# Kernel optimization log

Measured on AMD Instinct MI355X. Metric: run time of the kernel, lower is better.

The kernel has to match this reference:

```python
import jax, jax.numpy as jnp
import numpy as np

IGNORE_THR = 0.6
CONF_THR = 0.5
MAX_OBJ = 50


def iou(gx, gy, gl, gw, bx, by, bl, bw):
    # Faithful translation of get_ious (broadcastable).
    min_x = jnp.minimum(gx - gl / 2.0, bx - bl / 2.0)
    max_x = jnp.maximum(gx + gl / 2.0, bx + bl / 2.0)
    min_y = jnp.minimum(gy - gw / 2.0, by - bw / 2.0)
    max_y = jnp.maximum(gy + gw / 2.0, by + bw / 2.0)
    union_w = max_y - min_y
    union_h = max_x - min_x
    inter_w = gw + bw - union_w
    inter_l = gl + bl - union_h
    inter = jnp.where((inter_w <= 0) | (inter_l <= 0), 0.0, inter_w * inter_l)
    union = gw * gl + bw * bl - inter
    return inter / union


def build_targets(targets, fmap_preds, anchors, H, W, C):
    B, O, _ = targets.shape
    A = anchors.shape[0]
    # object loop breaks at first class==0 -> cumulative validity
    valid_all = jnp.cumprod((targets[:, :, 0] != 0).astype(jnp.int32), axis=1).astype(bool)  # [B,O]
    bidx = jnp.arange(B)
    aidx = jnp.arange(A)
    ch = jnp.arange(7 + C)

    def step(carry, xs):
        mask, conf, ts, n_gt, n_cor = carry
        t, valid = xs  # t: [B,7], valid: [B]
        gx = t[:, 1] * H
        gy = t[:, 2] * W
        gl = t[:, 3] * H
        gw = t[:, 4] * W
        # anchor matching: centered boxes (0,0,gl,gw) vs (0,0,al,aw) -> [B,A]
        ious = iou(0.0, 0.0, gl[:, None], gw[:, None],
                   0.0, 0.0, anchors[None, :, 0], anchors[None, :, 1])
        a = jnp.argmax(ious, axis=1)
        ax = gx.astype(jnp.int32)
        ay = gy.astype(jnp.int32)
        # conf_mask[b, ious>ign, ax, ay] = 0
        cur = conf[bidx[:, None], aidx[None, :], ax[:, None], ay[:, None]]  # [B,A]
        conf = conf.at[bidx[:, None], aidx[None, :], ax[:, None], ay[:, None]].set(
            jnp.where(valid[:, None] & (ious > IGNORE_THR), False, cur))
        # conf_mask[b, a, ax, ay] = 1 ; mask[b, a, ax, ay] = 1
        conf = conf.at[bidx, a, ax, ay].set(jnp.where(valid, True, conf[bidx, a, ax, ay]))
        mask = mask.at[bidx, a, ax, ay].set(jnp.where(valid, True, mask[bidx, a, ax, ay]))
        vals7 = jnp.stack([gx - ax, gy - ay,
                           jnp.log(gl / anchors[a, 0]), jnp.log(gw / anchors[a, 1]),
                           t[:, 5], t[:, 6], jnp.ones_like(gx)], axis=1)  # [B,7]
        cur_ts = ts[bidx, a, ax, ay]  # [B,7+C]
        cls_id = t[:, 0].astype(jnp.int32)
        new_ts = jnp.where(ch[None, :] < 7,
                           jnp.concatenate([vals7, jnp.zeros((B, C), vals7.dtype)], axis=1),
                           jnp.where(ch[None, :] == 7 + cls_id[:, None], 1.0, cur_ts))
        ts = ts.at[bidx, a, ax, ay].set(jnp.where(valid[:, None], new_ts, cur_ts))
        # statistics
        pred = fmap_preds[bidx, a, ax, ay]  # [B,8]
        piou = iou(gx, gy, gl, gw, pred[:, 0], pred[:, 1], pred[:, 2], pred[:, 3])
        correct = valid & (piou > 0.5) & (pred[:, 6] > CONF_THR)
        return (mask, conf, ts,
                n_gt + valid.astype(jnp.int32).sum(),
                n_cor + correct.astype(jnp.int32).sum()), None

    init = (jnp.zeros((B, A, H, W), bool), jnp.ones((B, A, H, W), bool),
            jnp.zeros((B, A, H, W, 7 + C), jnp.float32), jnp.int32(0), jnp.int32(0))
    xs = (jnp.swapaxes(targets, 0, 1), jnp.swapaxes(valid_all, 0, 1))
    (mask, conf, ts, n_gt, n_cor), _ = jax.lax.scan(step, init, xs)
    # torch uint8: false_mask = conf_mask - mask, truthy iff conf_mask != mask (wraps to 255)
    false_mask = conf != mask
    return ts, mask, false_mask, n_gt, n_cor


def region_loss(output, targets, anchors):
    B, _, H, W = output.shape
    A = anchors.shape[0]
    C = output.shape[1] // A - 7
    out = output.reshape(B, A, 7 + C, H, W).transpose(0, 1, 3, 4, 2)  # [B,A,H,W,7+C]
    o_x = jax.nn.sigmoid(out[..., 0])
    o_y = jax.nn.sigmoid(out[..., 1])
    o_l = out[..., 2]
    o_w = out[..., 3]
    o_im = out[..., 4]
    o_re = out[..., 5]
    o_conf = jax.nn.sigmoid(out[..., 6])
    o_cls = jax.nn.sigmoid(out[..., 7:])

    # get_fmap_prediction: c_x[h,w]=h, c_y[h,w]=w
    c_x = jnp.arange(H, dtype=out.dtype)[None, None, :, None]
    c_y = jnp.arange(W, dtype=out.dtype)[None, None, None, :]
    p_l = anchors[None, :, None, None, 0]
    p_w = anchors[None, :, None, None, 1]
    cls_scalar = jnp.argmax(o_cls).astype(out.dtype)  # scalar, as in original
    fmap_preds = jnp.stack([
        o_x + c_x, o_y + c_y,
        jnp.exp(o_l) * p_l, jnp.exp(o_w) * p_w,
        o_im, o_re, o_conf,
        jnp.broadcast_to(cls_scalar, o_x.shape)], axis=-1)  # [B,A,H,W,8]

    ts, mask, false_mask, n_gt, n_cor = build_targets(
        jax.lax.stop_gradient(targets),
        jax.lax.stop_gradient(fmap_preds),
        jax.lax.stop_gradient(anchors), H, W, C)
    ts = jax.lax.stop_gradient(ts)

    m = mask.astype(out.dtype)
    fm = false_mask.astype(out.dtype)
    nt = jnp.sum(m)
    nf = jnp.sum(fm)

    def mmse(o, t):
        return jnp.sum(m * (o - t) ** 2) / nt

    def bce(p, t, w, n):
        lp = jnp.clip(jnp.log(p), -100.0)
        ln = jnp.clip(jnp.log(1.0 - p), -100.0)
        return jnp.sum(w * -(t * lp + (1.0 - t) * ln)) / n

    loss_x = mmse(o_x, ts[..., 0])
    loss_y = mmse(o_y, ts[..., 1])
    loss_l = mmse(o_l, ts[..., 2])
    loss_w = mmse(o_w, ts[..., 3])
    loss_im = mmse(o_im, ts[..., 4])
    loss_re = mmse(o_re, ts[..., 5])
    loss_conf = bce(o_conf, ts[..., 6], fm, nf) + bce(o_conf, ts[..., 6], m, nt)
    labels = jnp.argmax(ts[..., 7:], axis=-1)
    ce = jax.nn.logsumexp(o_cls, axis=-1) - jnp.take_along_axis(o_cls, labels[..., None], axis=-1)[..., 0]
    loss_cls = (1.0 / B) * jnp.sum(m * ce) / nt
    loss = loss_x + loss_y + loss_w + loss_l + loss_im + loss_re + loss_conf + loss_cls
    return loss, n_gt, n_cor


def setup_inputs() -> dict:
    B, A, C, H, W, O = 32, 5, 8, 96, 96, MAX_OBJ
    key = jax.random.key(0)
    k1, k2, k3, k4, k5, k6 = jax.random.split(key, 6)
    output = jax.random.normal(k1, (B, A * (7 + C), H, W), dtype=jnp.float32)
    cls_all = jax.random.randint(k2, (B, O), 1, C).astype(jnp.float32)
    n_obj = jax.random.randint(k3, (B,), 5, O)
    cls_col = jnp.where(jnp.arange(O)[None, :] < n_obj[:, None], cls_all, 0.0)
    xy = jax.random.uniform(k4, (B, O, 2), minval=0.0, maxval=1.0)
    lw = jax.random.uniform(k5, (B, O, 2), minval=0.02, maxval=0.5)
    imre = jax.random.uniform(k6, (B, O, 2), minval=-1.0, maxval=1.0)
    targets = jnp.concatenate([cls_col[..., None], xy, lw, imre], axis=-1).astype(jnp.float32)
    anchors = jnp.asarray([[1.08, 1.19], [3.42, 4.41], [6.63, 11.38],
                           [9.42, 5.11], [16.62, 10.52]], dtype=jnp.float32)
    return {"output": output, "targets": targets, "anchors": anchors}


def reference(output, targets, anchors):
    return region_loss(output, targets, anchors)
```

## Files before the change

kernel.cpp:

```cpp
#include <hip/hip_runtime.h>

#define Bn 32
#define An 5
#define Cn 8
#define Hn 96
#define Wn 96
#define On 50
#define CHn 15
#define HWn (Hn*Wn)
#define NCELL (Bn*An*HWn)
#define NQ (NCELL/4)
#define QPP (HWn/4)

#define NBLK_D 224
#define GRID1 (Bn + NBLK_D)

#define OFF_BPART 0
#define OFF_PART  (Bn*13*4)

__device__ __forceinline__ float sigmoidf_(float x) { return 1.0f / (1.0f + expf(-x)); }
__device__ __forceinline__ float sp100(float v) {
    return fminf(log1pf(expf(v)), 100.0f);
}

__device__ __forceinline__ float iou_ref(float gx, float gy, float gl, float gw,
                                         float bx, float by, float bl, float bw) {
    float min_x = fminf(gx - gl * 0.5f, bx - bl * 0.5f);
    float max_x = fmaxf(gx + gl * 0.5f, bx + bl * 0.5f);
    float min_y = fminf(gy - gw * 0.5f, by - bw * 0.5f);
    float max_y = fmaxf(gy + gw * 0.5f, by + bw * 0.5f);
    float union_w = max_y - min_y;
    float union_h = max_x - min_x;
    float inter_w = gw + bw - union_w;
    float inter_l = gl + bl - union_h;
    float inter = (inter_w <= 0.0f || inter_l <= 0.0f) ? 0.0f : inter_w * inter_l;
    float uni = gw * gl + bw * bl - inter;
    return inter / uni;
}

__global__ __launch_bounds__(256) void k_main(const float* __restrict__ outp,
                                              const float* __restrict__ tgt,
                                              const float* __restrict__ anch,
                                              float* __restrict__ bpart,
                                              float* __restrict__ partials) {
    const int blk = blockIdx.x;
    const int tid = threadIdx.x;

    if (blk >= Bn) {
        float s = 0.0f;
        for (int q = (blk - Bn) * 256 + tid; q < NQ; q += NBLK_D * 256) {
            int plane = q / QPP;
            int r = q - plane * QPP;
            const float4 v = *(const float4*)(outp + ((size_t)plane * CHn + 6) * HWn + (size_t)r * 4);
            s += sp100(v.x) + sp100(v.y) + sp100(v.z) + sp100(v.w);
        }
        __shared__ float red[256];
        red[tid] = s;
        __syncthreads();
        for (int off = 128; off > 0; off >>= 1) {
            if (tid < off) red[tid] += red[tid + off];
            __syncthreads();
        }
        if (tid == 0) partials[blk - Bn] = red[0];
        return;
    }

    if (tid >= 64) return;
    const int b = blk;
    const int o = tid;

    float anv[10];
    #pragma unroll
    for (int k = 0; k < 10; ++k) anv[k] = anch[k];

    const float* t = tgt + (size_t)(b * On + o) * 7;
    float t0 = (o < On) ? t[0] : 0.0f;
    unsigned long long vm = __ballot(t0 != 0.0f);
    int nv = __ffsll(~vm) - 1;
    bool valid = o < nv;

    int best = 0, ign = 0, cellxy = -1, cls = 0;
    float ef0 = 0, ef1 = 0, ef2 = 0, ef3 = 0, ef4 = 0, ef5 = 0;
    float o0 = 0, o1 = 0, o2 = 0, o3 = 0, o4 = 0, o5 = 0, o6 = 0;
    bool correct = false;
    if (valid) {
        float gx = t[1] * (float)Hn, gy = t[2] * (float)Wn;
        float gl = t[3] * (float)Hn, gw = t[4] * (float)Wn;
        float bi = -1.0f, al = anv[0], aw = anv[1];
        #pragma unroll
        for (int a = 0; a < An; ++a) {
            float ia = iou_ref(0.0f, 0.0f, gl, gw, 0.0f, 0.0f, anv[2 * a], anv[2 * a + 1]);
            if (ia > bi) { bi = ia; best = a; al = anv[2 * a]; aw = anv[2 * a + 1]; }
            if (ia > 0.6f) ign |= (1 << a);
        }
        int ax = (int)gx, ay = (int)gy;
        cellxy = ax * Wn + ay;
        ef0 = gx - (float)ax;
        ef1 = gy - (float)ay;
        ef2 = logf(gl / al);
        ef3 = logf(gw / aw);
        ef4 = t[5];
        ef5 = t[6];
        cls = (int)t0;
        const float* p = outp + ((size_t)(b * An + best) * CHn) * HWn + cellxy;
        o0 = p[0]; o1 = p[HWn]; o2 = p[2 * HWn]; o3 = p[3 * HWn];
        o4 = p[4 * HWn]; o5 = p[5 * HWn]; o6 = p[6 * HWn];
        float px = sigmoidf_(o0) + (float)ax;
        float py = sigmoidf_(o1) + (float)ay;
        float pl = expf(o2) * al;
        float pw = expf(o3) * aw;
        float pc = sigmoidf_(o6);
        float piou = iou_ref(gx, gy, gl, gw, px, py, pl, pw);
        correct = (piou > 0.5f) && (pc > 0.5f);
    }
    int ncor = __popcll(__ballot(correct));

    int keyt = best * HWn + cellxy;
    bool has_later = false, has_earlier = false;
    int clsmin = cls, cbits = 0x1F, mbits = 0;
    for (int j = 0; j < nv; ++j) {
        int jc = __shfl(cellxy, j);
        int jb = __shfl(best, j);
        int ji = __shfl(ign, j);
        int jcl = __shfl(cls, j);
        if (valid) {
            if (jb * HWn + jc == keyt) {
                if (j > o) has_later = true;
                clsmin = min(clsmin, jcl);
            }
            if (jc == cellxy) {
                if (j < o) has_earlier = true;
                cbits = (cbits & ~ji) | (1 << jb);
                mbits |= (1 << jb);
            }
        }
    }
    bool is_last = valid && !has_later;
    bool is_leader = valid && !has_earlier;
    int cnt = __popcll(__ballot(is_last));

    float s0 = 0, s1 = 0, s2 = 0, s3 = 0, s4 = 0, s5 = 0, s6 = 0, s7 = 0;
    if (is_last) {
        float d;
        d = sigmoidf_(o0) - ef0; s0 = d * d;
        d = sigmoidf_(o1) - ef1; s1 = d * d;
        d = o2 - ef2;            s2 = d * d;
        d = o3 - ef3;            s3 = d * d;
        d = o4 - ef4;            s4 = d * d;
        d = o5 - ef5;            s5 = d * d;
        s6 = sp100(-o6);
        const float* p = outp + ((size_t)(b * An + best) * CHn) * HWn + cellxy;
        float sc[Cn], mx = -1e30f;
        #pragma unroll
        for (int k = 0; k < Cn; ++k) {
            sc[k] = sigmoidf_(p[(7 + k) * HWn]);
            mx = fmaxf(mx, sc[k]);
        }
        float se = 0.0f, sct = 0.0f;
        #pragma unroll
        for (int k = 0; k < Cn; ++k) {
            se += expf(sc[k] - mx);
            if (k == clsmin) sct = sc[k];
        }
        s7 = mx + logf(se) - sct;
    }

    float bcorr = 0.0f, nfcorr = 0.0f;
    if (is_leader) {
        const float* pc6 = outp + ((size_t)(b * An) * CHn + 6) * HWn + cellxy;
        #pragma unroll
        for (int a = 0; a < An; ++a) {
            int c = (cbits >> a) & 1, m = (mbits >> a) & 1;
            if (c == m) {
                float v = pc6[(size_t)a * CHn * HWn];
                bcorr -= sp100(v);
                nfcorr -= 1.0f;
            } else if (m == 1) {
                float v = pc6[(size_t)a * CHn * HWn];
                bcorr += sp100(-v) - sp100(v);
            }
        }
    }

    float r[10] = {s0, s1, s2, s3, s4, s5, s6, s7, bcorr, nfcorr};
    #pragma unroll
    for (int off = 32; off > 0; off >>= 1) {
        #pragma unroll
        for (int k = 0; k < 10; ++k) r[k] += __shfl_down(r[k], off);
    }
    if (o == 0) {
        float* dst = bpart + b * 13;
        #pragma unroll
        for (int k = 0; k < 10; ++k) dst[k] = r[k];
        dst[10] = (float)nv;
        dst[11] = (float)ncor;
        dst[12] = (float)cnt;
    }
}

__global__ __launch_bounds__(256) void k_final(const float* __restrict__ partials,
                                               const float* __restrict__ bpart,
                                               float* __restrict__ op) {
    int tid = threadIdx.x;
    float a0 = (tid < NBLK_D) ? partials[tid] : 0.0f;
    __shared__ float red[256];
    __shared__ float ds[13];
    if (tid < 13) {
        float s = 0.0f;
        for (int b = 0; b < Bn; ++b) s += bpart[b * 13 + tid];
        ds[tid] = s;
    }
    red[tid] = a0;
    __syncthreads();
    for (int off = 128; off > 0; off >>= 1) {
        if (tid < off) red[tid] += red[tid + off];
        __syncthreads();
    }
    if (tid == 0) {
        float fmbce = red[0] + ds[8];
        float nf = (float)NCELL + ds[9];
        float nt = ds[12];
        float loss_conf = fmbce / nf + ds[6] / nt;
        float loss_cls = (1.0f / (float)Bn) * ds[7] / nt;
        float loss = (ds[0] + ds[1] + ds[3] + ds[2] + ds[4] + ds[5]) / nt
                     + loss_conf + loss_cls;
        op[0] = loss;
        op[1] = ds[10];
        op[2] = ds[11];
    }
}

extern "C" void kernel_launch(void* const* d_in, const int* in_sizes, int n_in,
                              void* d_out, int out_size, void* d_ws, size_t ws_size,
                              hipStream_t stream) {
    const float* outp = (const float*)d_in[0];
    const float* tgt  = (const float*)d_in[1];
    const float* anch = (const float*)d_in[2];
    char* ws = (char*)d_ws;
    float* bpart = (float*)(ws + OFF_BPART);
    float* partials = (float*)(ws + OFF_PART);
    float* op = (float*)d_out;

    hipLaunchKernelGGL(k_main, dim3(GRID1), dim3(256), 0, stream,
                       outp, tgt, anch, bpart, partials);
    hipLaunchKernelGGL(k_final, dim3(1), dim3(256), 0, stream, partials, bpart, op);
}
```

Before: 19.08 us.

## Fuse main and final kernels into one cooperative launch with grid sync

Merges the two-kernel sequence into a single cooperative kernel. Blocks publish their partial results with agent-scope stores, and block 0 does the final reduction after a grid-wide barrier. This removes the second kernel launch and its inter-kernel gap. The per-object path also loads all 15 channels and the 5 anchor confidences up front instead of conditionally, trading extra loads for better latency hiding. Cooperative launch and the grid barrier add their own overhead.

```diff
diff --git a/kernel.cpp b/kernel.cpp
--- a/kernel.cpp
+++ b/kernel.cpp
@@ -1,4 +1,7 @@
 #include <hip/hip_runtime.h>
+#include <hip/hip_cooperative_groups.h>
+
+namespace cg = cooperative_groups;
 
 #define Bn 32
 #define An 5
@@ -21,6 +24,12 @@
 __device__ __forceinline__ float sigmoidf_(float x) { return 1.0f / (1.0f + expf(-x)); }
 __device__ __forceinline__ float sp100(float v) {
     return fminf(log1pf(expf(v)), 100.0f);
+}
+__device__ __forceinline__ void st_agent(float* p, float v) {
+    __hip_atomic_store(p, v, __ATOMIC_RELAXED, __HIP_MEMORY_SCOPE_AGENT);
+}
+__device__ __forceinline__ float ld_agent(const float* p) {
+    return __hip_atomic_load(p, __ATOMIC_RELAXED, __HIP_MEMORY_SCOPE_AGENT);
 }
 
 __device__ __forceinline__ float iou_ref(float gx, float gy, float gl, float gw,
@@ -38,13 +47,16 @@
     return inter / uni;
 }
 
-__global__ __launch_bounds__(256) void k_main(const float* __restrict__ outp,
-                                              const float* __restrict__ tgt,
-                                              const float* __restrict__ anch,
-                                              float* __restrict__ bpart,
-                                              float* __restrict__ partials) {
+__global__ __launch_bounds__(256) void k_all(const float* __restrict__ outp,
+                                             const float* __restrict__ tgt,
+                                             const float* __restrict__ anch,
+                                             float* __restrict__ bpart,
+                                             float* __restrict__ partials,
+                                             float* __restrict__ op) {
     const int blk = blockIdx.x;
     const int tid = threadIdx.x;
+    __shared__ float red[256];
+    __shared__ float ds[13];
 
     if (blk >= Bn) {
         float s = 0.0f;
@@ -54,179 +66,177 @@
             const float4 v = *(const float4*)(outp + ((size_t)plane * CHn + 6) * HWn + (size_t)r * 4);
             s += sp100(v.x) + sp100(v.y) + sp100(v.z) + sp100(v.w);
         }
-        __shared__ float red[256];
         red[tid] = s;
         __syncthreads();
         for (int off = 128; off > 0; off >>= 1) {
             if (tid < off) red[tid] += red[tid + off];
             __syncthreads();
         }
-        if (tid == 0) partials[blk - Bn] = red[0];
-        return;
+        if (tid == 0) st_agent(&partials[blk - Bn], red[0]);
+    } else if (tid < 64) {
+        const int b = blk;
+        const int o = tid;
+
+        float anv[10];
+        #pragma unroll
+        for (int k = 0; k < 10; ++k) anv[k] = anch[k];
+
+        const float* t = tgt + (size_t)(b * On + o) * 7;
+        float t0 = (o < On) ? t[0] : 0.0f;
+        unsigned long long vm = __ballot(t0 != 0.0f);
+        int nv = __ffsll(~vm) - 1;
+        bool valid = o < nv;
+
+        int best = 0, ign = 0, cellxy = -1, cls = 0;
+        float ef0 = 0, ef1 = 0, ef2 = 0, ef3 = 0, ef4 = 0, ef5 = 0;
+        float ch[CHn];
+        float va[An];
+        #pragma unroll
+        for (int k = 0; k < CHn; ++k) ch[k] = 0.0f;
+        #pragma unroll
+        for (int a = 0; a < An; ++a) va[a] = 0.0f;
+        bool correct = false;
+        if (valid) {
+            float gx = t[1] * (float)Hn, gy = t[2] * (float)Wn;
+            float gl = t[3] * (float)Hn, gw = t[4] * (float)Wn;
+            float bi = -1.0f, al = anv[0], aw = anv[1];
+            #pragma unroll
+            for (int a = 0; a < An; ++a) {
+                float ia = iou_ref(0.0f, 0.0f, gl, gw, 0.0f, 0.0f, anv[2 * a], anv[2 * a + 1]);
+                if (ia > bi) { bi = ia; best = a; al = anv[2 * a]; aw = anv[2 * a + 1]; }
+                if (ia > 0.6f) ign |= (1 << a);
+            }
+            int ax = (int)gx, ay = (int)gy;
+            cellxy = ax * Wn + ay;
+            ef0 = gx - (float)ax;
+            ef1 = gy - (float)ay;
+            ef2 = logf(gl / al);
+            ef3 = logf(gw / aw);
+            ef4 = t[5];
+            ef5 = t[6];
+            cls = (int)t0;
+            const float* p = outp + ((size_t)(b * An + best) * CHn) * HWn + cellxy;
+            #pragma unroll
+            for (int k = 0; k < CHn; ++k) ch[k] = p[(size_t)k * HWn];
+            const float* pc6 = outp + ((size_t)(b * An) * CHn + 6) * HWn + cellxy;
+            #pragma unroll
+            for (int a = 0; a < An; ++a) va[a] = pc6[(size_t)a * CHn * HWn];
+            float px = sigmoidf_(ch[0]) + (float)ax;
+            float py = sigmoidf_(ch[1]) + (float)ay;
+            float pl = expf(ch[2]) * al;
+            float pw = expf(ch[3]) * aw;
+            float pc = sigmoidf_(ch[6]);
+            float piou = iou_ref(gx, gy, gl, gw, px, py, pl, pw);
+            correct = (piou > 0.5f) && (pc > 0.5f);
+        }
+        int ncor = __popcll(__ballot(correct));
+
+        int keyt = best * HWn + cellxy;
+        bool has_later = false, has_earlier = false;
+        int clsmin = cls, cbits = 0x1F, mbits = 0;
+        for (int j = 0; j < nv; ++j) {
+            int jc = __shfl(cellxy, j);
+            int jb = __shfl(best, j);
+            int ji = __shfl(ign, j);
+            int jcl = __shfl(cls, j);
+            if (valid) {
+                if (jb * HWn + jc == keyt) {
+                    if (j > o) has_later = true;
+                    clsmin = min(clsmin, jcl);
+                }
+                if (jc == cellxy) {
+                    if (j < o) has_earlier = true;
+                    cbits = (cbits & ~ji) | (1 << jb);
+                    mbits |= (1 << jb);
+                }
+            }
+        }
+        bool is_last = valid && !has_later;
+        bool is_leader = valid && !has_earlier;
+        int cnt = __popcll(__ballot(is_last));
+
+        float s0 = 0, s1 = 0, s2 = 0, s3 = 0, s4 = 0, s5 = 0, s6 = 0, s7 = 0;
+        if (is_last) {
+            float d;
+            d = sigmoidf_(ch[0]) - ef0; s0 = d * d;
+            d = sigmoidf_(ch[1]) - ef1; s1 = d * d;
+            d = ch[2] - ef2;            s2 = d * d;
+            d = ch[3] - ef3;            s3 = d * d;
+            d = ch[4] - ef4;            s4 = d * d;
+            d = ch[5] - ef5;            s5 = d * d;
+            s6 = sp100(-ch[6]);
+            float sc[Cn], mx = -1e30f;
+            #pragma unroll
+            for (int k = 0; k < Cn; ++k) {
+                sc[k] = sigmoidf_(ch[7 + k]);
+                mx = fmaxf(mx, sc[k]);
+            }
+            float se = 0.0f, sct = 0.0f;
+            #pragma unroll
+            for (int k = 0; k < Cn; ++k) {
+                se += expf(sc[k] - mx);
+                if (k == clsmin) sct = sc[k];
+            }
+            s7 = mx + logf(se) - sct;
+        }
+
+        float bcorr = 0.0f, nfcorr = 0.0f;
+        if (is_leader) {
+            #pragma unroll
+            for (int a = 0; a < An; ++a) {
+                int c = (cbits >> a) & 1, m = (mbits >> a) & 1;
+                if (c == m) {
+                    bcorr -= sp100(va[a]);
+                    nfcorr -= 1.0f;
+                } else if (m == 1) {
+                    bcorr += sp100(-va[a]) - sp100(va[a]);
+                }
+            }
+        }
+
+        float r[10] = {s0, s1, s2, s3, s4, s5, s6, s7, bcorr, nfcorr};
+        #pragma unroll
+        for (int off = 32; off > 0; off >>= 1) {
+            #pragma unroll
+            for (int k = 0; k < 10; ++k) r[k] += __shfl_down(r[k], off);
+        }
+        if (o == 0) {
+            float* dst = bpart + b * 13;
+            #pragma unroll
+            for (int k = 0; k < 10; ++k) st_agent(&dst[k], r[k]);
+            st_agent(&dst[10], (float)nv);
+            st_agent(&dst[11], (float)ncor);
+            st_agent(&dst[12], (float)cnt);
+        }
     }
 
-    if (tid >= 64) return;
-    const int b = blk;
-    const int o = tid;
-
-    float anv[10];
-    #pragma unroll
-    for (int k = 0; k < 10; ++k) anv[k] = anch[k];
-
-    const float* t = tgt + (size_t)(b * On + o) * 7;
-    float t0 = (o < On) ? t[0] : 0.0f;
-    unsigned long long vm = __ballot(t0 != 0.0f);
-    int nv = __ffsll(~vm) - 1;
-    bool valid = o < nv;
-
-    int best = 0, ign = 0, cellxy = -1, cls = 0;
-    float ef0 = 0, ef1 = 0, ef2 = 0, ef3 = 0, ef4 = 0, ef5 = 0;
-    float o0 = 0, o1 = 0, o2 = 0, o3 = 0, o4 = 0, o5 = 0, o6 = 0;
-    bool correct = false;
-    if (valid) {
-        float gx = t[1] * (float)Hn, gy = t[2] * (float)Wn;
-        float gl = t[3] * (float)Hn, gw = t[4] * (float)Wn;
-        float bi = -1.0f, al = anv[0], aw = anv[1];
-        #pragma unroll
-        for (int a = 0; a < An; ++a) {
-            float ia = iou_ref(0.0f, 0.0f, gl, gw, 0.0f, 0.0f, anv[2 * a], anv[2 * a + 1]);
-            if (ia > bi) { bi = ia; best = a; al = anv[2 * a]; aw = anv[2 * a + 1]; }
-            if (ia > 0.6f) ign |= (1 << a);
-        }
-        int ax = (int)gx, ay = (int)gy;
-        cellxy = ax * Wn + ay;
-        ef0 = gx - (float)ax;
-        ef1 = gy - (float)ay;
-        ef2 = logf(gl / al);
-        ef3 = logf(gw / aw);
-        ef4 = t[5];
-        ef5 = t[6];
-        cls = (int)t0;
-        const float* p = outp + ((size_t)(b * An + best) * CHn) * HWn + cellxy;
-        o0 = p[0]; o1 = p[HWn]; o2 = p[2 * HWn]; o3 = p[3 * HWn];
-        o4 = p[4 * HWn]; o5 = p[5 * HWn]; o6 = p[6 * HWn];
-        float px = sigmoidf_(o0) + (float)ax;
-        float py = sigmoidf_(o1) + (float)ay;
-        float pl = expf(o2) * al;
-        float pw = expf(o3) * aw;
-        float pc = sigmoidf_(o6);
-        float piou = iou_ref(gx, gy, gl, gw, px, py, pl, pw);
-        correct = (piou > 0.5f) && (pc > 0.5f);
-    }
-    int ncor = __popcll(__ballot(correct));
-
-    int keyt = best * HWn + cellxy;
-    bool has_later = false, has_earlier = false;
-    int clsmin = cls, cbits = 0x1F, mbits = 0;
-    for (int j = 0; j < nv; ++j) {
-        int jc = __shfl(cellxy, j);
-        int jb = __shfl(best, j);
-        int ji = __shfl(ign, j);
-        int jcl = __shfl(cls, j);
-        if (valid) {
-            if (jb * HWn + jc == keyt) {
-                if (j > o) has_later = true;
-                clsmin = min(clsmin, jcl);
-            }
-            if (jc == cellxy) {
-                if (j < o) has_earlier = true;
-                cbits = (cbits & ~ji) | (1 << jb);
-                mbits |= (1 << jb);
-            }
-        }
-    }
-    bool is_last = valid && !has_later;
-    bool is_leader = valid && !has_earlier;
-    int cnt = __popcll(__ballot(is_last));
-
-    float s0 = 0, s1 = 0, s2 = 0, s3 = 0, s4 = 0, s5 = 0, s6 = 0, s7 = 0;
-    if (is_last) {
-        float d;
-        d = sigmoidf_(o0) - ef0; s0 = d * d;
-        d = sigmoidf_(o1) - ef1; s1 = d * d;
-        d = o2 - ef2;            s2 = d * d;
-        d = o3 - ef3;            s3 = d * d;
-        d = o4 - ef4;            s4 = d * d;
-        d = o5 - ef5;            s5 = d * d;
-        s6 = sp100(-o6);
-        const float* p = outp + ((size_t)(b * An + best) * CHn) * HWn + cellxy;
-        float sc[Cn], mx = -1e30f;
-        #pragma unroll
-        for (int k = 0; k < Cn; ++k) {
-            sc[k] = sigmoidf_(p[(7 + k) * HWn]);
-            mx = fmaxf(mx, sc[k]);
-        }
-        float se = 0.0f, sct = 0.0f;
-        #pragma unroll
-        for (int k = 0; k < Cn; ++k) {
-            se += expf(sc[k] - mx);
-            if (k == clsmin) sct = sc[k];
-        }
-        s7 = mx + logf(se) - sct;
-    }
-
-    float bcorr = 0.0f, nfcorr = 0.0f;
-    if (is_leader) {
-        const float* pc6 = outp + ((size_t)(b * An) * CHn + 6) * HWn + cellxy;
-        #pragma unroll
-        for (int a = 0; a < An; ++a) {
-            int c = (cbits >> a) & 1, m = (mbits >> a) & 1;
-            if (c == m) {
-                float v = pc6[(size_t)a * CHn * HWn];
-                bcorr -= sp100(v);
-                nfcorr -= 1.0f;
-            } else if (m == 1) {
-                float v = pc6[(size_t)a * CHn * HWn];
-                bcorr += sp100(-v) - sp100(v);
-            }
-        }
-    }
-
-    float r[10] = {s0, s1, s2, s3, s4, s5, s6, s7, bcorr, nfcorr};
-    #pragma unroll
-    for (int off = 32; off > 0; off >>= 1) {
-        #pragma unroll
-        for (int k = 0; k < 10; ++k) r[k] += __shfl_down(r[k], off);
-    }
-    if (o == 0) {
-        float* dst = bpart + b * 13;
-        #pragma unroll
-        for (int k = 0; k < 10; ++k) dst[k] = r[k];
-        dst[10] = (float)nv;
-        dst[11] = (float)ncor;
-        dst[12] = (float)cnt;
-    }
-}
-
-__global__ __launch_bounds__(256) void k_final(const float* __restrict__ partials,
-                                               const float* __restrict__ bpart,
-                                               float* __restrict__ op) {
-    int tid = threadIdx.x;
-    float a0 = (tid < NBLK_D) ? partials[tid] : 0.0f;
-    __shared__ float red[256];
-    __shared__ float ds[13];
-    if (tid < 13) {
-        float s = 0.0f;
-        for (int b = 0; b < Bn; ++b) s += bpart[b * 13 + tid];
-        ds[tid] = s;
-    }
-    red[tid] = a0;
-    __syncthreads();
-    for (int off = 128; off > 0; off >>= 1) {
-        if (tid < off) red[tid] += red[tid + off];
+    cg::this_grid().sync();
+
+    if (blk == 0) {
+        float a0 = (tid < NBLK_D) ? ld_agent(&partials[tid]) : 0.0f;
+        if (tid < 13) {
+            float s = 0.0f;
+            for (int b = 0; b < Bn; ++b) s += ld_agent(&bpart[b * 13 + tid]);
+            ds[tid] = s;
+        }
+        red[tid] = a0;
         __syncthreads();
-    }
-    if (tid == 0) {
-        float fmbce = red[0] + ds[8];
-        float nf = (float)NCELL + ds[9];
-        float nt = ds[12];
-        float loss_conf = fmbce / nf + ds[6] / nt;
-        float loss_cls = (1.0f / (float)Bn) * ds[7] / nt;
-        float loss = (ds[0] + ds[1] + ds[3] + ds[2] + ds[4] + ds[5]) / nt
-                     + loss_conf + loss_cls;
-        op[0] = loss;
-        op[1] = ds[10];
-        op[2] = ds[11];
+        for (int off = 128; off > 0; off >>= 1) {
+            if (tid < off) red[tid] += red[tid + off];
+            __syncthreads();
+        }
+        if (tid == 0) {
+            float fmbce = red[0] + ds[8];
+            float nf = (float)NCELL + ds[9];
+            float nt = ds[12];
+            float loss_conf = fmbce / nf + ds[6] / nt;
+            float loss_cls = (1.0f / (float)Bn) * ds[7] / nt;
+            float loss = (ds[0] + ds[1] + ds[3] + ds[2] + ds[4] + ds[5]) / nt
+                         + loss_conf + loss_cls;
+            op[0] = loss;
+            op[1] = ds[10];
+            op[2] = ds[11];
+        }
     }
 }
 
@@ -241,7 +251,8 @@
     float* partials = (float*)(ws + OFF_PART);
     float* op = (float*)d_out;
 
-    hipLaunchKernelGGL(k_main, dim3(GRID1), dim3(256), 0, stream,
-                       outp, tgt, anch, bpart, partials);
-    hipLaunchKernelGGL(k_final, dim3(1), dim3(256), 0, stream, partials, bpart, op);
-}
+    void* args[] = {(void*)&outp, (void*)&tgt, (void*)&anch,
+                    (void*)&bpart, (void*)&partials, (void*)&op};
+    hipLaunchCooperativeKernel((const void*)k_all, dim3(GRID1), dim3(256),
+                               args, 0, stream);
+}
```

After: 51.52 us. +170.1%, slower.
